# Kernel optimization log

Hardware: AMD Instinct MI355X
Metric: run time of the kernel (lower is better)

The kernel has to match this reference:

```python
import jax, jax.numpy as jnp
import numpy as np
from math import sqrt

SIZE = 4096
NR_CORES = 2
RANK = 16
D = 64  # core_size: D**NR_CORES == SIZE


def setup_inputs() -> dict:
    key = jax.random.key(0)
    k_x, k_c0, k_c1, k_b = jax.random.split(key, 4)
    t = 1.0 / sqrt(SIZE)
    sigma = (t * sqrt(RANK) ** (1 - NR_CORES)) ** (1.0 / NR_CORES)
    x = jax.random.normal(k_x, (2, 4096, SIZE), dtype=jnp.float32)
    core0 = sigma * jax.random.normal(k_c0, (D, D, D, RANK, 1), dtype=jnp.float32)
    core1 = sigma * jax.random.normal(k_c1, (D, D, D, 1, RANK), dtype=jnp.float32)
    bias = sqrt(1.0 / SIZE) * jax.random.uniform(k_b, (SIZE,), minval=-1.0, maxval=1.0, dtype=jnp.float32)
    return {"x": x, "core0": core0, "core1": core1, "bias": bias}


def _btt_forward(x, cores, bias):
    d, c, size = D, NR_CORES, SIZE
    G = cores[0]  # (d,...,d, r, 1)
    for idx, core in enumerate(cores[1:]):
        j = d ** (idx + 1)
        i = d ** (c - idx - 1)
        core_r = core.reshape(j, d, i, core.shape[-2], core.shape[-1])
        G_r = G.reshape(j, d ** (idx + 1), i, G.shape[-2], G.shape[-1])
        # contract rank dim b: (j,x,i,cb) x (j,y,i,ba) -> (j,x,y,i,c,a)
        G = jnp.einsum('jxicb,jyiba->jxyica', core_r, G_r)
    G = G.reshape(size, size)
    out = x.reshape(-1, size) @ G + bias
    return out.reshape(x.shape)


def reference(x, core0, core1, bias):
    return _btt_forward(x, [core0, core1], bias)
```

## Files before the change

kernel.cpp:

```cpp
#include <hip/hip_runtime.h>
#include <hip/hip_bf16.h>
#include <stdint.h>
#include <stddef.h>

using bf16 = __hip_bfloat16;

typedef __attribute__((ext_vector_type(4))) float f32x4;
typedef __attribute__((ext_vector_type(8))) short bf16x8;
typedef __attribute__((ext_vector_type(4))) unsigned short u16x4;

#define K_DIM 4096
#define M_ROWS 8192
#define BM 256
#define BN 256
#define BK 64
#define NT (K_DIM / BK)
#define NITER (NT / 2)
#define MT2 (M_ROWS / BM)
#define NT2 (K_DIM / BN)

template<bool B> struct BC { static constexpr bool value = B; };

__global__ void conv_bf16(const float* __restrict__ in, bf16* __restrict__ outb, int n4) {
  int idx = blockIdx.x * blockDim.x + threadIdx.x;
  int stride = gridDim.x * blockDim.x;
  for (int k = idx; k < n4; k += stride) {
    f32x4 v = ((const f32x4*)in)[k];
    bf16 tmp[4];
    tmp[0] = __float2bfloat16(v.x);
    tmp[1] = __float2bfloat16(v.y);
    tmp[2] = __float2bfloat16(v.z);
    tmp[3] = __float2bfloat16(v.w);
    ((u16x4*)outb)[k] = *(const u16x4*)tmp;
  }
}

__global__ void build_gt(const float* __restrict__ core0, const float* __restrict__ core1,
                         bf16* __restrict__ GT) {
  int j = blockIdx.x >> 6;
  int i = blockIdx.x & 63;
  __shared__ float c0s[64][16];
  __shared__ float c1s[64][16];
  int t = threadIdx.x;
#pragma unroll
  for (int rep = 0; rep < 4; ++rep) {
    int idx = rep * 256 + t;
    int row = idx >> 4;
    int b = idx & 15;
    size_t base = ((size_t)(j * 64 + row) * 64 + i) * 16 + b;
    c1s[row][b] = core1[base];
    c0s[row][b] = core0[base];
  }
  __syncthreads();
  int x = t & 63;
  int ys = t >> 6;
  float r1[16];
#pragma unroll
  for (int b = 0; b < 16; ++b) r1[b] = c1s[x][b];
#pragma unroll
  for (int yy = 0; yy < 16; ++yy) {
    int y = ys * 16 + yy;
    float acc = 0.f;
#pragma unroll
    for (int b = 0; b < 16; ++b) acc += r1[b] * c0s[y][b];
    GT[((size_t)(y * 64 + i) << 12) + (size_t)(j * 64 + x)] = __float2bfloat16(acc);
  }
}

__device__ __forceinline__ void gload_lds16(const bf16* g, bf16* l) {
  __builtin_amdgcn_global_load_lds(
      (const __attribute__((address_space(1))) unsigned int*)(g),
      (__attribute__((address_space(3))) unsigned int*)(l),
      16, 0, 0);
}

template<int MH>
__device__ __forceinline__ void read_a(bf16x8 (&af)[4][2], const bf16* As,
                                       int abase, int swk0, int swk1) {
#pragma unroll
  for (int mi = 0; mi < 4; ++mi) {
    int off = abase + (MH * 4 + mi) * 1024;
    af[mi][0] = *(const bf16x8*)&As[off + swk0];
    af[mi][1] = *(const bf16x8*)&As[off + swk1];
  }
}

template<int NH>
__device__ __forceinline__ void read_b(bf16x8 (&bfr)[4][2], const bf16* Bs,
                                       int bbase, int swk0, int swk1) {
#pragma unroll
  for (int ni = 0; ni < 2; ++ni) {
    int off = bbase + (NH * 2 + ni) * 1024;
    bfr[NH * 2 + ni][0] = *(const bf16x8*)&Bs[off + swk0];
    bfr[NH * 2 + ni][1] = *(const bf16x8*)&Bs[off + swk1];
  }
}

template<int MH, int NH>
__device__ __forceinline__ void mfma_quad(f32x4 (&acc)[8][4], const bf16x8 (&af)[4][2],
                                          const bf16x8 (&bfr)[4][2]) {
#pragma unroll
  for (int mi = 0; mi < 4; ++mi)
#pragma unroll
    for (int ni = 0; ni < 2; ++ni)
#pragma unroll
      for (int kk = 0; kk < 2; ++kk)
        acc[MH * 4 + mi][NH * 2 + ni] = __builtin_amdgcn_mfma_f32_16x16x32_bf16(
            af[mi][kk], bfr[NH * 2 + ni][kk], acc[MH * 4 + mi][NH * 2 + ni], 0, 0, 0);
}

#define BARRIER() __builtin_amdgcn_s_barrier()
#define SP1() __builtin_amdgcn_s_setprio(1)
#define SP0() __builtin_amdgcn_s_setprio(0)
#define VMCNT4() asm volatile("s_waitcnt vmcnt(4)" ::: "memory")
#define VMCNT0() asm volatile("s_waitcnt vmcnt(0)" ::: "memory")

__global__ __launch_bounds__(512, 2)
void gemm_xg(const bf16* __restrict__ Xb, const bf16* __restrict__ GT,
             const float* __restrict__ bias, float* __restrict__ out) {
  __shared__ bf16 As[2][BM * BK];
  __shared__ bf16 Bs[2][BN * BK];

  int bid = blockIdx.x;
  int sb = (bid & 7) * (MT2 * NT2 / 8) + (bid >> 3);
  int bm = sb >> 4;
  int bn = sb & 15;

  int t = threadIdx.x;
  int lane = t & 63;
  int wid = t >> 6;

  int srow = t >> 3;
  int scol = t & 7;
  int sxor = scol ^ (srow & 7);
  const bf16* gA0 = Xb + ((size_t)(bm * BM + srow) * K_DIM) + sxor * 8;
  const bf16* gB0 = GT + ((size_t)(bn * BN + srow) * K_DIM) + sxor * 8;
  int lbase = srow * BK + scol * 8;

  auto sA = [&](int buf, int h, int kt) {
    const bf16* g = gA0 + (size_t)(h * 128) * K_DIM + (size_t)kt * BK;
    bf16* l = &As[buf][h * 128 * BK + lbase];
    gload_lds16(g, l);
    gload_lds16(g + (size_t)64 * K_DIM, l + 64 * BK);
  };
  auto sB = [&](int buf, int h, int kt) {
    const bf16* g = gB0 + (size_t)(h * 128) * K_DIM + (size_t)kt * BK;
    bf16* l = &Bs[buf][h * 128 * BK + lbase];
    gload_lds16(g, l);
    gload_lds16(g + (size_t)64 * K_DIM, l + 64 * BK);
  };

  int wm = wid >> 2;
  int wn = wid & 3;
  int lr = lane & 15;
  int g4 = lane >> 4;
  int x7 = lr & 7;
  int swk0 = ((g4 ^ x7) << 3);
  int swk1 = (((4 + g4) ^ x7) << 3);
  int abase = (wm * 128 + lr) * BK;
  int bbase = (wn * 64 + lr) * BK;

  f32x4 acc[8][4] = {};
  bf16x8 af[4][2];
  bf16x8 bfr[4][2];

  const bf16* A0 = &As[0][0];
  const bf16* B0 = &Bs[0][0];
  const bf16* A1 = &As[1][0];
  const bf16* B1 = &Bs[1][0];

  sA(0, 0, 0); sA(0, 1, 0);
  sB(0, 0, 0); sB(0, 1, 0);
  sB(1, 0, 1); sB(1, 1, 1);
  VMCNT4();
  BARRIER();

  auto run_iter = [&](int i, auto lastc) {
    constexpr bool LAST = decltype(lastc)::value;
    const int t1 = 2 * i + 1, t2 = 2 * i + 2, t3 = 2 * i + 3;

    VMCNT4();
    read_a<0>(af, A0, abase, swk0, swk1);
    read_b<0>(bfr, B0, bbase, swk0, swk1);
    sA(1, 0, t1);
    BARRIER(); SP1(); mfma_quad<0, 0>(acc, af, bfr); SP0(); BARRIER();

    read_b<1>(bfr, B0, bbase, swk0, swk1);
    sA(1, 1, t1);
    BARRIER(); SP1(); mfma_quad<0, 1>(acc, af, bfr); SP0(); BARRIER();

    read_a<1>(af, A0, abase, swk0, swk1);
    if (!LAST) sB(0, 0, t2);
    BARRIER(); SP1(); mfma_quad<1, 0>(acc, af, bfr); SP0(); BARRIER();

    if (!LAST) sB(0, 1, t2);
    BARRIER(); SP1(); mfma_quad<1, 1>(acc, af, bfr); SP0(); BARRIER();

    if (!LAST) { VMCNT4(); } else { VMCNT0(); }
    read_a<0>(af, A1, abase, swk0, swk1);
    read_b<0>(bfr, B1, bbase, swk0, swk1);
    if (!LAST) sA(0, 0, t2);
    BARRIER(); SP1(); mfma_quad<0, 0>(acc, af, bfr); SP0(); BARRIER();

    read_b<1>(bfr, B1, bbase, swk0, swk1);
    if (!LAST) sA(0, 1, t2);
    BARRIER(); SP1(); mfma_quad<0, 1>(acc, af, bfr); SP0(); BARRIER();

    read_a<1>(af, A1, abase, swk0, swk1);
    if (!LAST) sB(1, 0, t3);
    BARRIER(); SP1(); mfma_quad<1, 0>(acc, af, bfr); SP0(); BARRIER();

    if (!LAST) sB(1, 1, t3);
    BARRIER(); SP1(); mfma_quad<1, 1>(acc, af, bfr); SP0(); BARRIER();
  };

#pragma unroll 1
  for (int i = 0; i < NITER - 1; ++i) run_iter(i, BC<false>{});
  run_iter(NITER - 1, BC<true>{});

  int colbase = bn * BN + wn * 64 + lr;
  int rowbase = bm * BM + wm * 128 + g4 * 4;
#pragma unroll
  for (int ni = 0; ni < 4; ++ni) {
    int col = colbase + ni * 16;
    float bv = bias[col];
#pragma unroll
    for (int mi = 0; mi < 8; ++mi) {
#pragma unroll
      for (int r = 0; r < 4; ++r) {
        int row = rowbase + mi * 16 + r;
        out[(size_t)row * K_DIM + col] = acc[mi][ni][r] + bv;
      }
    }
  }
}

extern "C" void kernel_launch(void* const* d_in, const int* in_sizes, int n_in,
                              void* d_out, int out_size, void* d_ws, size_t ws_size,
                              hipStream_t stream) {
  const float* x     = (const float*)d_in[0];
  const float* core0 = (const float*)d_in[1];
  const float* core1 = (const float*)d_in[2];
  const float* bias  = (const float*)d_in[3];
  float* out = (float*)d_out;

  bf16* Xb = (bf16*)d_ws;
  bf16* GT = (bf16*)((char*)d_ws + (size_t)M_ROWS * K_DIM * sizeof(bf16));

  conv_bf16<<<2048, 256, 0, stream>>>(x, Xb, (M_ROWS * K_DIM) / 4);
  build_gt<<<4096, 256, 0, stream>>>(core0, core1, GT);
  gemm_xg<<<MT2 * NT2, 512, 0, stream>>>(Xb, GT, bias, out);
}
```

Baseline: 288.3 us.

## Restructure GEMM main loop into per-tile stages with two barriers per tile

```diff
diff --git a/kernel.cpp b/kernel.cpp
--- a/kernel.cpp
+++ b/kernel.cpp
@@ -15,11 +15,10 @@
 #define BN 256
 #define BK 64
 #define NT (K_DIM / BK)
-#define NITER (NT / 2)
 #define MT2 (M_ROWS / BM)
 #define NT2 (K_DIM / BN)
 
-template<bool B> struct BC { static constexpr bool value = B; };
+template<int M> struct MC { static constexpr int value = M; };
 
 __global__ void conv_bf16(const float* __restrict__ in, bf16* __restrict__ outb, int n4) {
   int idx = blockIdx.x * blockDim.x + threadIdx.x;
@@ -164,59 +163,43 @@
   bf16x8 af[4][2];
   bf16x8 bfr[4][2];
 
+  auto tile = [&](int kt, const bf16* Ab, const bf16* Bb, int obuf, int cbuf, auto mode) {
+    constexpr int MODE = decltype(mode)::value;
+    if (MODE == 2) { VMCNT0(); } else { VMCNT4(); }
+    BARRIER();
+    if (MODE < 2) { sA(obuf, 0, kt + 1); sA(obuf, 1, kt + 1); }
+    read_a<0>(af, Ab, abase, swk0, swk1);
+    read_b<0>(bfr, Bb, bbase, swk0, swk1);
+    read_b<1>(bfr, Bb, bbase, swk0, swk1);
+    SP1();
+    mfma_quad<0, 0>(acc, af, bfr);
+    mfma_quad<0, 1>(acc, af, bfr);
+    SP0();
+    read_a<1>(af, Ab, abase, swk0, swk1);
+    SP1();
+    mfma_quad<1, 0>(acc, af, bfr);
+    mfma_quad<1, 1>(acc, af, bfr);
+    SP0();
+    BARRIER();
+    if (MODE == 0) { sB(cbuf, 0, kt + 2); sB(cbuf, 1, kt + 2); }
+  };
+
   const bf16* A0 = &As[0][0];
   const bf16* B0 = &Bs[0][0];
   const bf16* A1 = &As[1][0];
   const bf16* B1 = &Bs[1][0];
 
+  sB(0, 0, 0); sB(0, 1, 0);
   sA(0, 0, 0); sA(0, 1, 0);
-  sB(0, 0, 0); sB(0, 1, 0);
   sB(1, 0, 1); sB(1, 1, 1);
-  VMCNT4();
-  BARRIER();
-
-  auto run_iter = [&](int i, auto lastc) {
-    constexpr bool LAST = decltype(lastc)::value;
-    const int t1 = 2 * i + 1, t2 = 2 * i + 2, t3 = 2 * i + 3;
-
-    VMCNT4();
-    read_a<0>(af, A0, abase, swk0, swk1);
-    read_b<0>(bfr, B0, bbase, swk0, swk1);
-    sA(1, 0, t1);
-    BARRIER(); SP1(); mfma_quad<0, 0>(acc, af, bfr); SP0(); BARRIER();
-
-    read_b<1>(bfr, B0, bbase, swk0, swk1);
-    sA(1, 1, t1);
-    BARRIER(); SP1(); mfma_quad<0, 1>(acc, af, bfr); SP0(); BARRIER();
-
-    read_a<1>(af, A0, abase, swk0, swk1);
-    if (!LAST) sB(0, 0, t2);
-    BARRIER(); SP1(); mfma_quad<1, 0>(acc, af, bfr); SP0(); BARRIER();
-
-    if (!LAST) sB(0, 1, t2);
-    BARRIER(); SP1(); mfma_quad<1, 1>(acc, af, bfr); SP0(); BARRIER();
-
-    if (!LAST) { VMCNT4(); } else { VMCNT0(); }
-    read_a<0>(af, A1, abase, swk0, swk1);
-    read_b<0>(bfr, B1, bbase, swk0, swk1);
-    if (!LAST) sA(0, 0, t2);
-    BARRIER(); SP1(); mfma_quad<0, 0>(acc, af, bfr); SP0(); BARRIER();
-
-    read_b<1>(bfr, B1, bbase, swk0, swk1);
-    if (!LAST) sA(0, 1, t2);
-    BARRIER(); SP1(); mfma_quad<0, 1>(acc, af, bfr); SP0(); BARRIER();
-
-    read_a<1>(af, A1, abase, swk0, swk1);
-    if (!LAST) sB(1, 0, t3);
-    BARRIER(); SP1(); mfma_quad<1, 0>(acc, af, bfr); SP0(); BARRIER();
-
-    if (!LAST) sB(1, 1, t3);
-    BARRIER(); SP1(); mfma_quad<1, 1>(acc, af, bfr); SP0(); BARRIER();
-  };
 
 #pragma unroll 1
-  for (int i = 0; i < NITER - 1; ++i) run_iter(i, BC<false>{});
-  run_iter(NITER - 1, BC<true>{});
+  for (int i = 0; i < NT / 2 - 1; ++i) {
+    tile(2 * i,     A0, B0, 1, 0, MC<0>{});
+    tile(2 * i + 1, A1, B1, 0, 1, MC<0>{});
+  }
+  tile(NT - 2, A0, B0, 1, 0, MC<1>{});
+  tile(NT - 1, A1, B1, 0, 1, MC<2>{});
 
   int colbase = bn * BN + wn * 64 + lr;
   int rowbase = bm * BM + wm * 128 + g4 * 4;
```

Result: slower. 297.4 us (+3.2%).
